# Kernel tuning notes

Measured on AMD Instinct MI355X. Metric: run time of the kernel, lower is better.

## Reference

```python
import jax, jax.numpy as jnp
import numpy as np

T, B, D, H = 512, 64, 1024, 1024


def setup_inputs() -> dict:
    key = jax.random.key(0)
    ks = jax.random.split(key, 7)
    stdv = 1.0 / np.sqrt(H)
    u = lambda k, shape: jax.random.uniform(k, shape, jnp.float32, -stdv, stdv)
    return {
        "x": jax.random.normal(ks[0], (T, B, D), jnp.float32),
        "h0": jax.random.normal(ks[1], (B, H), jnp.float32),
        "c0": jax.random.normal(ks[2], (B, H), jnp.float32),
        "w_ih": u(ks[3], (4 * H, D)),
        "b_ih": u(ks[4], (4 * H,)),
        "w_hh": u(ks[5], (4 * H, H)),
        "b_hh": u(ks[6], (4 * H,)),
    }


def reference(x, h0, c0, w_ih, b_ih, w_hh, b_hh):
    # Precompute input projection for all timesteps in one big GEMM: [T,B,4H]
    gates_x = jnp.einsum("tbd,gd->tbg", x, w_ih) + b_ih

    def step(carry, gx_t):
        h, c = carry
        gates = gx_t + h @ w_hh.T + b_hh  # [B, 4H]
        i_in, f_in, g_in, o_in = jnp.split(gates, 4, axis=1)
        i_t = jax.nn.sigmoid(i_in)
        f_t = jax.nn.sigmoid(f_in)
        g_t = jnp.tanh(g_in)
        o_t = jax.nn.sigmoid(o_in)
        c_t = f_t * c + i_t * g_t
        h_t = o_t * jnp.tanh(c_t)
        return (h_t, c_t), h_t

    (h_n, c_n), hs = jax.lax.scan(step, (h0, c0), gates_x)
    # output: [T, B, H]; final states: [B, H]
    return hs, h_n, c_n
```

## Files before the change

### kernel.cpp

```cpp
#include <hip/hip_runtime.h>

#define TT 512
#define NB 64
#define DD 1024
#define NG 4096

typedef __attribute__((ext_vector_type(8))) __bf16 bf16x8;
typedef __attribute__((ext_vector_type(4))) float f32x4;

#define WC_OFF   0ul
#define HBUF_OFF 16777216ul
#define BIAS_OFF (HBUF_OFF + 262144ul)
#define CNT_OFF  (BIAS_OFF + 16384ul)
#define XBF_OFF  (CNT_OFF + 8192ul)
#define WS_FULL  (XBF_OFF + 67108864ul)

__device__ __forceinline__ unsigned short f2bf(float f) {
  unsigned int u = __float_as_uint(f);
  u += 0x7fffu + ((u >> 16) & 1u);
  return (unsigned short)(u >> 16);
}

__global__ void prep_kernel(const float* __restrict__ x, const float* __restrict__ h0,
                            const float* __restrict__ w_ih, const float* __restrict__ b_ih,
                            const float* __restrict__ w_hh, const float* __restrict__ b_hh,
                            unsigned char* __restrict__ ws, int use_xbf) {
  unsigned short* Wc  = (unsigned short*)(ws + WC_OFF);
  unsigned short* hb  = (unsigned short*)(ws + HBUF_OFF);
  float* bias         = (float*)(ws + BIAS_OFF);
  int* cnt            = (int*)(ws + CNT_OFF);
  unsigned short* xbf = (unsigned short*)(ws + XBF_OFF);
  long tid = (long)blockIdx.x * blockDim.x + threadIdx.x;
  long stride = (long)gridDim.x * blockDim.x;
  for (long i = tid; i < (long)NG * 2048; i += stride) {
    int r = (int)(i >> 11), k = (int)(i & 2047);
    float v = (k < 1024) ? w_ih[(long)r * 1024 + k] : w_hh[(long)r * 1024 + (k - 1024)];
    Wc[i] = f2bf(v);
  }
  for (long i = tid; i < NG; i += stride) bias[i] = b_ih[i] + b_hh[i];
  for (long i = tid; i < NB * DD; i += stride) hb[65536 + i] = f2bf(h0[i]);
  for (long i = tid; i < 4 * TT; i += stride) cnt[i] = 0;
  if (use_xbf) {
    for (long i = tid; i < (long)TT * NB * DD; i += stride) xbf[i] = f2bf(x[i]);
  }
}

#define MFMA16 __builtin_amdgcn_mfma_f32_16x16x32_bf16

__launch_bounds__(512, 2)
__global__ void lstm_kernel(const float* __restrict__ x, const float* __restrict__ c0,
                            float* __restrict__ out, unsigned char* __restrict__ ws,
                            int use_xbf) {
  __shared__ __align__(16) float red[2][8][16][68];
  __shared__ float bias_l[64];

  const unsigned short* Wc   = (const unsigned short*)(ws + WC_OFF);
  unsigned long long* hb64   = (unsigned long long*)(ws + HBUF_OFF);
  const float* bias          = (const float*)(ws + BIAS_OFF);
  int* flags                 = (int*)(ws + CNT_OFF);
  const unsigned short* xbf  = (const unsigned short*)(ws + XBF_OFF);

  const int tid = threadIdx.x;
  const int bg = blockIdx.x >> 6;
  const int cg = blockIdx.x & 63;
  const int m0 = bg << 4;
  const int j0 = cg << 4;
  const int wv = tid >> 6;
  const int lane = tid & 63;
  const int ln = lane & 15;
  const int lq = lane >> 4;

  bf16x8 wx[16], wh[16];
  {
    const int kx = wv * 128 + lq * 8;
#pragma unroll
    for (int g = 0; g < 4; ++g) {
      const unsigned short* wp = Wc + (long)(g * 1024 + j0 + ln) * 2048 + kx;
#pragma unroll
      for (int ks = 0; ks < 4; ++ks) {
        wx[g * 4 + ks] = *reinterpret_cast<const bf16x8*>(wp + ks * 32);
        wh[g * 4 + ks] = *reinterpret_cast<const bf16x8*>(wp + 1024 + ks * 32);
      }
    }
  }
  if (tid < 64) bias_l[tid] = bias[(tid >> 4) * 1024 + j0 + (tid & 15)];

  const int mm = lane >> 2;
  const int jj0 = (lane & 3) << 2;
  float cr0 = 0.f, cr1 = 0.f, cr2 = 0.f, cr3 = 0.f;
  if (wv == 0) {
    const float4 cv = *(const float4*)(c0 + (long)(m0 + mm) * DD + j0 + jj0);
    cr0 = cv.x; cr1 = cv.y; cr2 = cv.z; cr3 = cv.w;
  }

  const long xbase = (long)(m0 + ln) * DD + wv * 128 + lq * 8;
  uint4 xcur[4];
  auto load_x = [&](int tt) {
    if (use_xbf) {
      const unsigned short* xp = xbf + (long)tt * (NB * DD) + xbase;
#pragma unroll
      for (int ks = 0; ks < 4; ++ks)
        xcur[ks] = *reinterpret_cast<const uint4*>(xp + ks * 32);
    } else {
      const float* xp = x + (long)tt * (NB * DD) + xbase;
#pragma unroll
      for (int ks = 0; ks < 4; ++ks) {
        float4 f0 = *reinterpret_cast<const float4*>(xp + ks * 32);
        float4 f1 = *reinterpret_cast<const float4*>(xp + ks * 32 + 4);
        uint4 pk;
        pk.x = (unsigned)f2bf(f0.x) | ((unsigned)f2bf(f0.y) << 16);
        pk.y = (unsigned)f2bf(f0.z) | ((unsigned)f2bf(f0.w) << 16);
        pk.z = (unsigned)f2bf(f1.x) | ((unsigned)f2bf(f1.y) << 16);
        pk.w = (unsigned)f2bf(f1.z) | ((unsigned)f2bf(f1.w) << 16);
        xcur[ks] = pk;
      }
    }
  };
  load_x(0);

  const int fl0 = (bg * 64 + wv * 8 + (lane & 7)) * 8;
  const int myflag = (bg * 64 + cg) * 8;
  const int hrow = (m0 + ln) * 256 + wv * 32 + lq * 2;

#pragma unroll 1
  for (int t = 0; t < TT; ++t) {
    const int rb = t & 1;

    if (t > 0) {
      while (true) {
        int v = __hip_atomic_load(flags + fl0, __ATOMIC_RELAXED, __HIP_MEMORY_SCOPE_AGENT);
        if (__all(v >= t)) break;
        __builtin_amdgcn_s_sleep(1);
      }
    }
    asm volatile("" ::: "memory");

    const unsigned long long* hp = hb64 + ((t + 1) & 1) * 16384 + hrow;
    unsigned long long hq[8];
#pragma unroll
    for (int ks = 0; ks < 4; ++ks) {
      hq[2 * ks]     = __hip_atomic_load(hp + ks * 8,     __ATOMIC_RELAXED, __HIP_MEMORY_SCOPE_AGENT);
      hq[2 * ks + 1] = __hip_atomic_load(hp + ks * 8 + 1, __ATOMIC_RELAXED, __HIP_MEMORY_SCOPE_AGENT);
    }

    f32x4 a0 = {0.f, 0.f, 0.f, 0.f}, a1 = a0, a2 = a0, a3 = a0;
#pragma unroll
    for (int ks = 0; ks < 4; ++ks) {
      bf16x8 af = __builtin_bit_cast(bf16x8, xcur[ks]);
      a0 = MFMA16(af, wx[ks],      a0, 0, 0, 0);
      a1 = MFMA16(af, wx[4 + ks],  a1, 0, 0, 0);
      a2 = MFMA16(af, wx[8 + ks],  a2, 0, 0, 0);
      a3 = MFMA16(af, wx[12 + ks], a3, 0, 0, 0);
    }
    if (wv != 0 && t + 1 < TT) load_x(t + 1);

#pragma unroll
    for (int ks = 0; ks < 4; ++ks) {
      union { unsigned long long q[2]; bf16x8 v; } uu;
      uu.q[0] = hq[2 * ks]; uu.q[1] = hq[2 * ks + 1];
      a0 = MFMA16(uu.v, wh[ks],      a0, 0, 0, 0);
      a1 = MFMA16(uu.v, wh[4 + ks],  a1, 0, 0, 0);
      a2 = MFMA16(uu.v, wh[8 + ks],  a2, 0, 0, 0);
      a3 = MFMA16(uu.v, wh[12 + ks], a3, 0, 0, 0);
    }

#pragma unroll
    for (int r = 0; r < 4; ++r) {
      float* rp = &red[rb][wv][lq * 4 + r][ln];
      rp[0] = a0[r]; rp[16] = a1[r]; rp[32] = a2[r]; rp[48] = a3[r];
    }

    asm volatile("s_waitcnt lgkmcnt(0)" ::: "memory");
    __builtin_amdgcn_s_barrier();
    __builtin_amdgcn_sched_barrier(0);

    if (wv == 0) {
      __builtin_amdgcn_s_setprio(1);
      f32x4 s0 = *(const f32x4*)&bias_l[jj0];
      f32x4 s1 = *(const f32x4*)&bias_l[16 + jj0];
      f32x4 s2 = *(const f32x4*)&bias_l[32 + jj0];
      f32x4 s3 = *(const f32x4*)&bias_l[48 + jj0];
#pragma unroll
      for (int w = 0; w < 8; ++w) {
        const float* rp = &red[rb][w][mm][jj0];
        s0 += *(const f32x4*)(rp);
        s1 += *(const f32x4*)(rp + 16);
        s2 += *(const f32x4*)(rp + 32);
        s3 += *(const f32x4*)(rp + 48);
      }
      float cold[4] = {cr0, cr1, cr2, cr3};
      float hv[4], cn[4];
#pragma unroll
      for (int e = 0; e < 4; ++e) {
        float ig = 1.f / (1.f + __expf(-s0[e]));
        float fg = 1.f / (1.f + __expf(-s1[e]));
        float gg = 1.f - 2.f / (__expf(2.f * s2[e]) + 1.f);
        float og = 1.f / (1.f + __expf(-s3[e]));
        float c2 = fg * cold[e] + ig * gg;
        cn[e] = c2;
        hv[e] = og * (1.f - 2.f / (__expf(2.f * c2) + 1.f));
      }
      cr0 = cn[0]; cr1 = cn[1]; cr2 = cn[2]; cr3 = cn[3];

      const long ho = (long)(m0 + mm) * 1024 + j0 + jj0;
      *(float4*)(out + (long)t * 65536 + ho) = make_float4(hv[0], hv[1], hv[2], hv[3]);
      if (t == TT - 1) {
        *(float4*)(out + (long)TT * 65536 + ho) = make_float4(hv[0], hv[1], hv[2], hv[3]);
        *(float4*)(out + (long)TT * 65536 + 65536 + ho) = make_float4(cn[0], cn[1], cn[2], cn[3]);
      }
      unsigned long long hqo = (unsigned long long)f2bf(hv[0])
        | ((unsigned long long)f2bf(hv[1]) << 16)
        | ((unsigned long long)f2bf(hv[2]) << 32)
        | ((unsigned long long)f2bf(hv[3]) << 48);
      __hip_atomic_store(hb64 + rb * 16384 + (m0 + mm) * 256 + ((j0 + jj0) >> 2), hqo,
                         __ATOMIC_RELAXED, __HIP_MEMORY_SCOPE_AGENT);
      asm volatile("s_waitcnt vmcnt(0)" ::: "memory");
      if (lane == 0)
        __hip_atomic_store(flags + myflag, t + 1, __ATOMIC_RELAXED, __HIP_MEMORY_SCOPE_AGENT);
      __builtin_amdgcn_s_setprio(0);
      if (t + 1 < TT) load_x(t + 1);
    }
  }
}

extern "C" void kernel_launch(void* const* d_in, const int* in_sizes, int n_in,
                              void* d_out, int out_size, void* d_ws, size_t ws_size,
                              hipStream_t stream) {
  const float* x    = (const float*)d_in[0];
  const float* h0   = (const float*)d_in[1];
  const float* c0   = (const float*)d_in[2];
  const float* w_ih = (const float*)d_in[3];
  const float* b_ih = (const float*)d_in[4];
  const float* w_hh = (const float*)d_in[5];
  const float* b_hh = (const float*)d_in[6];
  float* out = (float*)d_out;
  unsigned char* ws = (unsigned char*)d_ws;
  int use_xbf = (ws_size >= WS_FULL) ? 1 : 0;

  hipLaunchKernelGGL(prep_kernel, dim3(2048), dim3(256), 0, stream,
                     x, h0, w_ih, b_ih, w_hh, b_hh, ws, use_xbf);

  void* args[] = { (void*)&x, (void*)&c0, (void*)&out, (void*)&ws, (void*)&use_xbf };
  hipLaunchCooperativeKernel(reinterpret_cast<void*>(lstm_kernel),
                             dim3(256), dim3(512), args, 0, stream);
}
```

Measured before the change: 3.190 ms.

## Embed step tags in h words to replace flag polling, split epilogue across two waves

Drops the separate per-block flag array. Each 64-bit h-buffer word now carries two bf16 values plus the timestep in its upper half, so consumers spin directly on the data until every tag matches, instead of polling a flag and then reloading h. This removes the vmcnt wait and the separate flag store on the producer side. The gate epilogue now runs on two waves, each handling two columns, rather than one wave handling four. The cost is a doubled h-buffer footprint and twice as many atomic loads per poll.

```diff
diff --git a/kernel.cpp b/kernel.cpp
--- a/kernel.cpp
+++ b/kernel.cpp
@@ -9,10 +9,9 @@
 typedef __attribute__((ext_vector_type(4))) float f32x4;
 
 #define WC_OFF   0ul
-#define HBUF_OFF 16777216ul
-#define BIAS_OFF (HBUF_OFF + 262144ul)
-#define CNT_OFF  (BIAS_OFF + 16384ul)
-#define XBF_OFF  (CNT_OFF + 8192ul)
+#define HB2_OFF  16777216ul
+#define BIAS_OFF (HB2_OFF + 524288ul)
+#define XBF_OFF  (BIAS_OFF + 16384ul)
 #define WS_FULL  (XBF_OFF + 67108864ul)
 
 __device__ __forceinline__ unsigned short f2bf(float f) {
@@ -26,9 +25,8 @@
                             const float* __restrict__ w_hh, const float* __restrict__ b_hh,
                             unsigned char* __restrict__ ws, int use_xbf) {
   unsigned short* Wc  = (unsigned short*)(ws + WC_OFF);
-  unsigned short* hb  = (unsigned short*)(ws + HBUF_OFF);
+  unsigned long long* hb2 = (unsigned long long*)(ws + HB2_OFF);
   float* bias         = (float*)(ws + BIAS_OFF);
-  int* cnt            = (int*)(ws + CNT_OFF);
   unsigned short* xbf = (unsigned short*)(ws + XBF_OFF);
   long tid = (long)blockIdx.x * blockDim.x + threadIdx.x;
   long stride = (long)gridDim.x * blockDim.x;
@@ -38,8 +36,12 @@
     Wc[i] = f2bf(v);
   }
   for (long i = tid; i < NG; i += stride) bias[i] = b_ih[i] + b_hh[i];
-  for (long i = tid; i < NB * DD; i += stride) hb[65536 + i] = f2bf(h0[i]);
-  for (long i = tid; i < 4 * TT; i += stride) cnt[i] = 0;
+  for (long i = tid; i < (long)NB * 512; i += stride) {
+    int row = (int)(i >> 9), jc = (int)(i & 511);
+    const float* hp = h0 + (long)row * 1024 + jc * 2;
+    hb2[32768 + i] = (unsigned long long)f2bf(hp[0]) | ((unsigned long long)f2bf(hp[1]) << 16);
+    hb2[i] = 0ull;
+  }
   if (use_xbf) {
     for (long i = tid; i < (long)TT * NB * DD; i += stride) xbf[i] = f2bf(x[i]);
   }
@@ -55,9 +57,8 @@
   __shared__ float bias_l[64];
 
   const unsigned short* Wc   = (const unsigned short*)(ws + WC_OFF);
-  unsigned long long* hb64   = (unsigned long long*)(ws + HBUF_OFF);
+  unsigned long long* hb2    = (unsigned long long*)(ws + HB2_OFF);
   const float* bias          = (const float*)(ws + BIAS_OFF);
-  int* flags                 = (int*)(ws + CNT_OFF);
   const unsigned short* xbf  = (const unsigned short*)(ws + XBF_OFF);
 
   const int tid = threadIdx.x;
@@ -85,12 +86,12 @@
   }
   if (tid < 64) bias_l[tid] = bias[(tid >> 4) * 1024 + j0 + (tid & 15)];
 
-  const int mm = lane >> 2;
-  const int jj0 = (lane & 3) << 2;
-  float cr0 = 0.f, cr1 = 0.f, cr2 = 0.f, cr3 = 0.f;
-  if (wv == 0) {
-    const float4 cv = *(const float4*)(c0 + (long)(m0 + mm) * DD + j0 + jj0);
-    cr0 = cv.x; cr1 = cv.y; cr2 = cv.z; cr3 = cv.w;
+  const int rrow = ((wv & 1) << 3) + (lane >> 3);
+  const int jc   = lane & 7;
+  float cr0 = 0.f, cr1 = 0.f;
+  if (wv < 2) {
+    const float2 cv = *(const float2*)(c0 + (long)(m0 + rrow) * DD + j0 + 2 * jc);
+    cr0 = cv.x; cr1 = cv.y;
   }
 
   const long xbase = (long)(m0 + ln) * DD + wv * 128 + lq * 8;
@@ -118,29 +119,27 @@
   };
   load_x(0);
 
-  const int fl0 = (bg * 64 + wv * 8 + (lane & 7)) * 8;
-  const int myflag = (bg * 64 + cg) * 8;
-  const int hrow = (m0 + ln) * 256 + wv * 32 + lq * 2;
+  const int hrow = (m0 + ln) * 512 + wv * 64 + lq * 4;
 
 #pragma unroll 1
   for (int t = 0; t < TT; ++t) {
     const int rb = t & 1;
 
-    if (t > 0) {
-      while (true) {
-        int v = __hip_atomic_load(flags + fl0, __ATOMIC_RELAXED, __HIP_MEMORY_SCOPE_AGENT);
-        if (__all(v >= t)) break;
-        __builtin_amdgcn_s_sleep(1);
-      }
-    }
-    asm volatile("" ::: "memory");
-
-    const unsigned long long* hp = hb64 + ((t + 1) & 1) * 16384 + hrow;
-    unsigned long long hq[8];
-#pragma unroll
-    for (int ks = 0; ks < 4; ++ks) {
-      hq[2 * ks]     = __hip_atomic_load(hp + ks * 8,     __ATOMIC_RELAXED, __HIP_MEMORY_SCOPE_AGENT);
-      hq[2 * ks + 1] = __hip_atomic_load(hp + ks * 8 + 1, __ATOMIC_RELAXED, __HIP_MEMORY_SCOPE_AGENT);
+    const unsigned long long* hp = hb2 + (((t + 1) & 1) << 15) + hrow;
+    const unsigned tgt = (unsigned)t;
+    unsigned long long q[16];
+    while (true) {
+#pragma unroll
+      for (int ks = 0; ks < 4; ++ks)
+#pragma unroll
+        for (int u = 0; u < 4; ++u)
+          q[ks * 4 + u] = __hip_atomic_load(hp + ks * 16 + u,
+                                            __ATOMIC_RELAXED, __HIP_MEMORY_SCOPE_AGENT);
+      bool ok = true;
+#pragma unroll
+      for (int i = 0; i < 16; ++i) ok &= ((unsigned)(q[i] >> 32) == tgt);
+      if (__all(ok)) break;
+      __builtin_amdgcn_s_sleep(1);
     }
 
     f32x4 a0 = {0.f, 0.f, 0.f, 0.f}, a1 = a0, a2 = a0, a3 = a0;
@@ -152,16 +151,20 @@
       a2 = MFMA16(af, wx[8 + ks],  a2, 0, 0, 0);
       a3 = MFMA16(af, wx[12 + ks], a3, 0, 0, 0);
     }
-    if (wv != 0 && t + 1 < TT) load_x(t + 1);
+    if (wv >= 2 && t + 1 < TT) load_x(t + 1);
 
 #pragma unroll
     for (int ks = 0; ks < 4; ++ks) {
-      union { unsigned long long q[2]; bf16x8 v; } uu;
-      uu.q[0] = hq[2 * ks]; uu.q[1] = hq[2 * ks + 1];
-      a0 = MFMA16(uu.v, wh[ks],      a0, 0, 0, 0);
-      a1 = MFMA16(uu.v, wh[4 + ks],  a1, 0, 0, 0);
-      a2 = MFMA16(uu.v, wh[8 + ks],  a2, 0, 0, 0);
-      a3 = MFMA16(uu.v, wh[12 + ks], a3, 0, 0, 0);
+      uint4 pk;
+      pk.x = (unsigned)q[ks * 4 + 0];
+      pk.y = (unsigned)q[ks * 4 + 1];
+      pk.z = (unsigned)q[ks * 4 + 2];
+      pk.w = (unsigned)q[ks * 4 + 3];
+      bf16x8 hf = __builtin_bit_cast(bf16x8, pk);
+      a0 = MFMA16(hf, wh[ks],      a0, 0, 0, 0);
+      a1 = MFMA16(hf, wh[4 + ks],  a1, 0, 0, 0);
+      a2 = MFMA16(hf, wh[8 + ks],  a2, 0, 0, 0);
+      a3 = MFMA16(hf, wh[12 + ks], a3, 0, 0, 0);
     }
 
 #pragma unroll
@@ -174,49 +177,47 @@
     __builtin_amdgcn_s_barrier();
     __builtin_amdgcn_sched_barrier(0);
 
-    if (wv == 0) {
+    if (wv < 2) {
       __builtin_amdgcn_s_setprio(1);
-      f32x4 s0 = *(const f32x4*)&bias_l[jj0];
-      f32x4 s1 = *(const f32x4*)&bias_l[16 + jj0];
-      f32x4 s2 = *(const f32x4*)&bias_l[32 + jj0];
-      f32x4 s3 = *(const f32x4*)&bias_l[48 + jj0];
+      float s00 = bias_l[2 * jc],      s01 = bias_l[2 * jc + 1];
+      float s10 = bias_l[16 + 2 * jc], s11 = bias_l[16 + 2 * jc + 1];
+      float s20 = bias_l[32 + 2 * jc], s21 = bias_l[32 + 2 * jc + 1];
+      float s30 = bias_l[48 + 2 * jc], s31 = bias_l[48 + 2 * jc + 1];
 #pragma unroll
       for (int w = 0; w < 8; ++w) {
-        const float* rp = &red[rb][w][mm][jj0];
-        s0 += *(const f32x4*)(rp);
-        s1 += *(const f32x4*)(rp + 16);
-        s2 += *(const f32x4*)(rp + 32);
-        s3 += *(const f32x4*)(rp + 48);
-      }
-      float cold[4] = {cr0, cr1, cr2, cr3};
-      float hv[4], cn[4];
-#pragma unroll
-      for (int e = 0; e < 4; ++e) {
-        float ig = 1.f / (1.f + __expf(-s0[e]));
-        float fg = 1.f / (1.f + __expf(-s1[e]));
-        float gg = 1.f - 2.f / (__expf(2.f * s2[e]) + 1.f);
-        float og = 1.f / (1.f + __expf(-s3[e]));
-        float c2 = fg * cold[e] + ig * gg;
-        cn[e] = c2;
-        hv[e] = og * (1.f - 2.f / (__expf(2.f * c2) + 1.f));
-      }
-      cr0 = cn[0]; cr1 = cn[1]; cr2 = cn[2]; cr3 = cn[3];
-
-      const long ho = (long)(m0 + mm) * 1024 + j0 + jj0;
-      *(float4*)(out + (long)t * 65536 + ho) = make_float4(hv[0], hv[1], hv[2], hv[3]);
+        const float* rp = &red[rb][w][rrow][2 * jc];
+        float2 v0 = *(const float2*)(rp);
+        float2 v1 = *(const float2*)(rp + 16);
+        float2 v2 = *(const float2*)(rp + 32);
+        float2 v3 = *(const float2*)(rp + 48);
+        s00 += v0.x; s01 += v0.y;
+        s10 += v1.x; s11 += v1.y;
+        s20 += v2.x; s21 += v2.y;
+        s30 += v3.x; s31 += v3.y;
+      }
+      float ig0 = 1.f / (1.f + __expf(-s00)), ig1 = 1.f / (1.f + __expf(-s01));
+      float fg0 = 1.f / (1.f + __expf(-s10)), fg1 = 1.f / (1.f + __expf(-s11));
+      float gg0 = 1.f - 2.f / (__expf(2.f * s20) + 1.f);
+      float gg1 = 1.f - 2.f / (__expf(2.f * s21) + 1.f);
+      float og0 = 1.f / (1.f + __expf(-s30)), og1 = 1.f / (1.f + __expf(-s31));
+      float cn0 = fg0 * cr0 + ig0 * gg0;
+      float cn1 = fg1 * cr1 + ig1 * gg1;
+      cr0 = cn0; cr1 = cn1;
+      float hv0 = og0 * (1.f - 2.f / (__expf(2.f * cn0) + 1.f));
+      float hv1 = og1 * (1.f - 2.f / (__expf(2.f * cn1) + 1.f));
+
+      unsigned long long pw = (unsigned long long)f2bf(hv0)
+        | ((unsigned long long)f2bf(hv1) << 16)
+        | ((unsigned long long)(unsigned)(t + 1) << 32);
+      __hip_atomic_store(hb2 + ((t & 1) << 15) + (m0 + rrow) * 512 + (j0 >> 1) + jc, pw,
+                         __ATOMIC_RELAXED, __HIP_MEMORY_SCOPE_AGENT);
+
+      const long ho = (long)(m0 + rrow) * 1024 + j0 + 2 * jc;
+      *(float2*)(out + (long)t * 65536 + ho) = make_float2(hv0, hv1);
       if (t == TT - 1) {
-        *(float4*)(out + (long)TT * 65536 + ho) = make_float4(hv[0], hv[1], hv[2], hv[3]);
-        *(float4*)(out + (long)TT * 65536 + 65536 + ho) = make_float4(cn[0], cn[1], cn[2], cn[3]);
-      }
-      unsigned long long hqo = (unsigned long long)f2bf(hv[0])
-        | ((unsigned long long)f2bf(hv[1]) << 16)
-        | ((unsigned long long)f2bf(hv[2]) << 32)
-        | ((unsigned long long)f2bf(hv[3]) << 48);
-      __hip_atomic_store(hb64 + rb * 16384 + (m0 + mm) * 256 + ((j0 + jj0) >> 2), hqo,
-                         __ATOMIC_RELAXED, __HIP_MEMORY_SCOPE_AGENT);
-      asm volatile("s_waitcnt vmcnt(0)" ::: "memory");
-      if (lane == 0)
-        __hip_atomic_store(flags + myflag, t + 1, __ATOMIC_RELAXED, __HIP_MEMORY_SCOPE_AGENT);
+        *(float2*)(out + (long)TT * 65536 + ho) = make_float2(hv0, hv1);
+        *(float2*)(out + (long)TT * 65536 + 65536 + ho) = make_float2(cn0, cn1);
+      }
       __builtin_amdgcn_s_setprio(0);
       if (t + 1 < TT) load_x(t + 1);
     }
```

Result: slower. 5.061 ms (+58.7%).
